# Performance work log

Hardware: AMD Instinct MI355X
Metric: run time of the kernel (lower is better)

## Reference

```python
import jax, jax.numpy as jnp
import numpy as np

D_CH = 2048  # channels
N = 64       # hidden_state
L = 8192     # sequence length
MIN_DELTA, MAX_DELTA = 1e-3, 0.1


def setup_inputs() -> dict:
    key = jax.random.key(0)
    ks = jax.random.split(key, 5)
    X = jax.random.normal(ks[0], (D_CH, L), jnp.float32)
    # kaiming_normal_(nonlinearity='linear'): std = 1/sqrt(fan_in=N)
    A = jax.random.normal(ks[1], (N, N), jnp.float32) * (1.0 / N) ** 0.5
    B = jax.random.normal(ks[2], (N, D_CH), jnp.float32) * (1.0 / N) ** 0.5
    C = jax.random.normal(ks[3], (D_CH, N), jnp.float32)
    Dp = jnp.ones((D_CH,), jnp.float32)
    log_delta = jax.random.uniform(ks[4], (1,), jnp.float32,
                                   float(np.log(MIN_DELTA)), float(np.log(MAX_DELTA)))
    return {"X": X, "A": A, "B": B, "C": C, "Dp": Dp, "log_delta": log_delta}


def reference(X, A, B, C, Dp, log_delta):
    # X: (D, L). Bilinear (Tustin) discretization with dt = exp(log_delta).
    n = A.shape[0]
    delta = jnp.exp(log_delta)[0]
    I = jnp.eye(n, dtype=A.dtype)
    inv = jnp.linalg.inv(I - (delta * 0.5) * A)
    dA = inv @ (I + (delta * 0.5) * A)      # (N, N)
    dB = delta * (inv @ B)                   # (N, D)

    def step(h, x_t):
        # h: (N,), x_t: (D,)
        h = dA @ h + dB @ x_t
        return h, C @ h                      # y_t: (D,)

    h0 = jnp.zeros((n,), X.dtype)
    _, ys = jax.lax.scan(step, h0, X.T)      # ys: (L, D)
    # skip connection y += D * X (per-channel)
    return ys.T + Dp[:, None] * X            # (D, L)
```

## Files before the change

### kernel.cpp

```cpp
#include <hip/hip_runtime.h>
#include <math.h>

#define D_CH 2048
#define LSEQ 8192
#define T1 32
#define NC1 256
#define VSLAB 524288

typedef __attribute__((ext_vector_type(8))) short bf16x8;
typedef __attribute__((ext_vector_type(4))) float f32x4;

__device__ __forceinline__ short f2bf(float x) {
  unsigned u = __float_as_uint(x);
  u += 0x7FFFu + ((u >> 16) & 1);
  return (short)(u >> 16);
}

__device__ __forceinline__ void mmzero(float acc[16]) {
#pragma unroll
  for (int t = 0; t < 16; ++t) acc[t] = 0.f;
}

template <int SZ>
__device__ __forceinline__ void mmld(float acc[16], const float* __restrict__ Z,
                                     int r0, int c0) {
#pragma unroll
  for (int i = 0; i < 4; ++i) {
    float4 z = *(const float4*)&Z[(r0 + i) * SZ + c0];
    acc[i * 4 + 0] = z.x; acc[i * 4 + 1] = z.y;
    acc[i * 4 + 2] = z.z; acc[i * 4 + 3] = z.w;
  }
}

template <int SX, int SY>
__device__ __forceinline__ void mac44(float acc[16], const float* __restrict__ Xb,
                                      const float* __restrict__ Yb, int r0, int c0) {
#pragma unroll 4
  for (int k = 0; k < 64; k += 4) {
    float4 x0 = *(const float4*)&Xb[(r0 + 0) * SX + k];
    float4 x1 = *(const float4*)&Xb[(r0 + 1) * SX + k];
    float4 x2 = *(const float4*)&Xb[(r0 + 2) * SX + k];
    float4 x3 = *(const float4*)&Xb[(r0 + 3) * SX + k];
    float4 y0 = *(const float4*)&Yb[(k + 0) * SY + c0];
    float4 y1 = *(const float4*)&Yb[(k + 1) * SY + c0];
    float4 y2 = *(const float4*)&Yb[(k + 2) * SY + c0];
    float4 y3 = *(const float4*)&Yb[(k + 3) * SY + c0];
#define MROW(i, xi) \
    acc[i * 4 + 0] += xi.x * y0.x + xi.y * y1.x + xi.z * y2.x + xi.w * y3.x; \
    acc[i * 4 + 1] += xi.x * y0.y + xi.y * y1.y + xi.z * y2.y + xi.w * y3.y; \
    acc[i * 4 + 2] += xi.x * y0.z + xi.y * y1.z + xi.z * y2.z + xi.w * y3.z; \
    acc[i * 4 + 3] += xi.x * y0.w + xi.y * y1.w + xi.z * y2.w + xi.w * y3.w;
    MROW(0, x0) MROW(1, x1) MROW(2, x2) MROW(3, x3)
#undef MROW
  }
}

template <int SZ>
__device__ __forceinline__ void mmst(float* Dst, const float acc[16], int r0, int c0) {
#pragma unroll
  for (int i = 0; i < 4; ++i)
    *(float4*)&Dst[(r0 + i) * SZ + c0] =
        make_float4(acc[i * 4 + 0], acc[i * 4 + 1], acc[i * 4 + 2], acc[i * 4 + 3]);
}

__global__ __launch_bounds__(256) void main_kernel(const float* __restrict__ X,
                                                   const float* __restrict__ A,
                                                   const float* __restrict__ B,
                                                   const float* __restrict__ logd,
                                                   float* __restrict__ invdT,
                                                   float* __restrict__ dAg,
                                                   float* __restrict__ V,
                                                   int KS) {
  __shared__ float smem[8704];
  const int tid = threadIdx.x;
  const int lane = tid & 63;
  const int w = tid >> 6;

  if (blockIdx.x == 0) {
    float* bQ = smem;
    float* bP = smem + 4352;
    const int r0 = (tid >> 4) * 4, c0 = (tid & 15) * 4;
    const float delta = expf(logd[0]);
    const float half = 0.5f * delta;
    float accQ[16], accP[16];

    for (int idx = tid; idx < 4096; idx += 256) {
      int i = idx >> 6, j = idx & 63;
      float p = half * A[idx];
      bP[i * 68 + j] = p;
      bQ[i * 68 + j] = p + (i == j ? 1.f : 0.f);
    }
    __syncthreads();
    mmzero(accP); mac44<68, 68>(accP, bP, bP, r0, c0);
    __syncthreads();
    mmst<68>(bP, accP, r0, c0);
    __syncthreads();
#pragma unroll 1
    for (int s = 0; s < 2; ++s) {
      mmld<68>(accQ, bQ, r0, c0);
      mac44<68, 68>(accQ, bP, bQ, r0, c0);
      if (s < 1) { mmzero(accP); mac44<68, 68>(accP, bP, bP, r0, c0); }
      __syncthreads();
      mmst<68>(bQ, accQ, r0, c0);
      if (s < 1) mmst<68>(bP, accP, r0, c0);
      __syncthreads();
    }

    for (int idx = tid; idx < 4096; idx += 256) {
      int n = idx >> 6, m = idx & 63;
      float qv = bQ[n * 68 + m];
      invdT[m * 64 + n] = delta * qv;
      dAg[idx] = 2.f * qv - (n == m ? 1.f : 0.f);
    }
    return;
  }

  const int b = blockIdx.x - 1;
  const int t0 = (b & 255) << 5;
  const int slab = b >> 8;
  const int k0 = slab * KS;
  short* Xs = (short*)smem;
  short* Bs = (short*)smem + 2432;
  const int q = lane >> 4, r = lane & 15;
  const int hi = lane >> 5, tl = lane & 31;
  const int brow = lane >> 3;
  const int bkc = (lane & 7) * 8;
  const int wm = (w & 1) * 16;
  const int wn = (w >> 1) * 32;

  f32x4 acc[2];
#pragma unroll
  for (int j = 0; j < 2; ++j) acc[j] = (f32x4){0.f, 0.f, 0.f, 0.f};

  float xv[8];
  float bv[16];

#define LOADX(KK)                                                              \
  _Pragma("unroll")                                                            \
  for (int j = 0; j < 8; ++j)                                                  \
    xv[j] = X[(size_t)(k0 + (KK) + w * 16 + hi * 8 + j) * LSEQ + t0 + tl];

#define LOADB(KK)                                                              \
  _Pragma("unroll")                                                            \
  for (int pp = 0; pp < 2; ++pp) {                                             \
    int n = pp * 32 + w * 8 + brow;                                            \
    float4 f0 = *(const float4*)&B[(size_t)n * D_CH + k0 + (KK) + bkc];        \
    float4 f1 = *(const float4*)&B[(size_t)n * D_CH + k0 + (KK) + bkc + 4];    \
    bv[pp * 8 + 0] = f0.x; bv[pp * 8 + 1] = f0.y;                              \
    bv[pp * 8 + 2] = f0.z; bv[pp * 8 + 3] = f0.w;                              \
    bv[pp * 8 + 4] = f1.x; bv[pp * 8 + 5] = f1.y;                              \
    bv[pp * 8 + 6] = f1.z; bv[pp * 8 + 7] = f1.w;                              \
  }

  LOADX(0)
  LOADB(0)

  for (int kk = 0; kk < KS; kk += 64) {
    bf16x8 xp;
#pragma unroll
    for (int j = 0; j < 8; ++j) xp[j] = f2bf(xv[j]);
    *(bf16x8*)&Xs[tl * 76 + w * 16 + hi * 8] = xp;
#pragma unroll
    for (int pp = 0; pp < 2; ++pp) {
      bf16x8 bp8;
#pragma unroll
      for (int j = 0; j < 8; ++j) bp8[j] = f2bf(bv[pp * 8 + j]);
      *(bf16x8*)&Bs[(pp * 32 + w * 8 + brow) * 76 + bkc] = bp8;
    }
    __syncthreads();

    if (kk + 64 < KS) {
      LOADX(kk + 64)
      LOADB(kk + 64)
    }

#pragma unroll
    for (int ks = 0; ks < 64; ks += 32) {
      bf16x8 a = *(const bf16x8*)&Xs[(wm + r) * 76 + ks + q * 8];
#pragma unroll
      for (int j = 0; j < 2; ++j) {
        bf16x8 bb = *(const bf16x8*)&Bs[(wn + j * 16 + r) * 76 + ks + q * 8];
        acc[j] = __builtin_amdgcn_mfma_f32_16x16x32_bf16(a, bb, acc[j], 0, 0, 0);
      }
    }
    __syncthreads();
  }
#undef LOADX
#undef LOADB

  float* Vs = V + (size_t)slab * VSLAB;
#pragma unroll
  for (int j = 0; j < 2; ++j)
#pragma unroll
    for (int reg = 0; reg < 4; ++reg)
      Vs[(size_t)(t0 + wm + q * 4 + reg) * 64 + wn + j * 16 + r] = acc[j][reg];
}

__device__ __forceinline__ float matvec_lds(const float* __restrict__ Mrow,
                                            const float* __restrict__ hb, float u) {
  float a0 = u, a1 = 0.f, a2 = 0.f, a3 = 0.f;
#pragma unroll
  for (int jj = 0; jj < 64; jj += 4) {
    float4 m = *(const float4*)&Mrow[jj];
    float4 hv = *(const float4*)&hb[jj];
    a0 += m.x * hv.x;
    a1 += m.y * hv.y;
    a2 += m.z * hv.z;
    a3 += m.w * hv.w;
  }
  return (a0 + a1) + (a2 + a3);
}

__device__ __forceinline__ void stage_mat64(float* Mlds, const float* __restrict__ Mg,
                                            int lane) {
#pragma unroll
  for (int i = 0; i < 16; ++i) {
    int row = i * 4 + (lane >> 4);
    int col = (lane & 15) * 4;
    *(float4*)&Mlds[row * 68 + col] = *(const float4*)&Mg[row * 64 + col];
  }
  __syncthreads();
}

__global__ __launch_bounds__(256) void scan1_kernel(const float* __restrict__ V,
                                                    const float* __restrict__ invdT,
                                                    const float* __restrict__ dA,
                                                    float* __restrict__ U,
                                                    float* __restrict__ S,
                                                    float* __restrict__ dA32g,
                                                    float* __restrict__ dA512g,
                                                    int nslab) {
  __shared__ float smem[13056];
  const int tid = threadIdx.x;
  const int c = blockIdx.x;

  if (c == NC1) {
    float* b0 = smem;
    float* b1 = smem + 4352;
    const int r0 = (tid >> 4) * 4, c0 = (tid & 15) * 4;
    for (int idx = tid; idx < 4096; idx += 256)
      b0[(idx >> 6) * 68 + (idx & 63)] = dA[idx];
    __syncthreads();
    float acc[16];
    float* p = b0; float* q = b1;
    for (int s = 1; s <= 9; ++s) {
      mmzero(acc); mac44<68, 68>(acc, p, p, r0, c0);
      if (s == 5) mmst<64>(dA32g, acc, r0, c0);
      if (s == 9) mmst<64>(dA512g, acc, r0, c0);
      mmst<68>(q, acc, r0, c0);
      __syncthreads();
      float* t = p; p = q; q = t;
    }
    return;
  }

  float* invs = smem;
  float* Vs   = smem + 4096;
  float* Us   = smem + 6144;
  float* hs0  = smem + 8192;
  float* hs1  = smem + 8256;
  float* Md   = smem + 8320;

  for (int idx = tid; idx < 4096; idx += 256) invs[idx] = invdT[idx];
  for (int idx = tid; idx < 4096; idx += 256)
    Md[(idx >> 6) * 68 + (idx & 63)] = dA[idx];
  for (int idx = tid; idx < 2048; idx += 256) {
    float v = 0.f;
    for (int s = 0; s < nslab; ++s) v += V[(size_t)s * VSLAB + (size_t)c * 2048 + idx];
    Vs[idx] = v;
  }
  __syncthreads();

  const int r0 = (tid >> 4) * 2, c0 = (tid & 15) * 4;
  float a0[4] = {0.f, 0.f, 0.f, 0.f}, a1[4] = {0.f, 0.f, 0.f, 0.f};
#pragma unroll 4
  for (int k = 0; k < 64; k += 4) {
    float4 v0 = *(const float4*)&Vs[r0 * 64 + k];
    float4 v1 = *(const float4*)&Vs[(r0 + 1) * 64 + k];
    float4 y0 = *(const float4*)&invs[(k + 0) * 64 + c0];
    float4 y1 = *(const float4*)&invs[(k + 1) * 64 + c0];
    float4 y2 = *(const float4*)&invs[(k + 2) * 64 + c0];
    float4 y3 = *(const float4*)&invs[(k + 3) * 64 + c0];
    a0[0] += v0.x * y0.x + v0.y * y1.x + v0.z * y2.x + v0.w * y3.x;
    a0[1] += v0.x * y0.y + v0.y * y1.y + v0.z * y2.y + v0.w * y3.y;
    a0[2] += v0.x * y0.z + v0.y * y1.z + v0.z * y2.z + v0.w * y3.z;
    a0[3] += v0.x * y0.w + v0.y * y1.w + v0.z * y2.w + v0.w * y3.w;
    a1[0] += v1.x * y0.x + v1.y * y1.x + v1.z * y2.x + v1.w * y3.x;
    a1[1] += v1.x * y0.y + v1.y * y1.y + v1.z * y2.y + v1.w * y3.y;
    a1[2] += v1.x * y0.z + v1.y * y1.z + v1.z * y2.z + v1.w * y3.z;
    a1[3] += v1.x * y0.w + v1.y * y1.w + v1.z * y2.w + v1.w * y3.w;
  }
  *(float4*)&Us[r0 * 64 + c0] = make_float4(a0[0], a0[1], a0[2], a0[3]);
  *(float4*)&Us[(r0 + 1) * 64 + c0] = make_float4(a1[0], a1[1], a1[2], a1[3]);
  *(float4*)&U[(size_t)(c * 32 + r0) * 64 + c0] = make_float4(a0[0], a0[1], a0[2], a0[3]);
  *(float4*)&U[(size_t)(c * 32 + r0 + 1) * 64 + c0] = make_float4(a1[0], a1[1], a1[2], a1[3]);
  __syncthreads();

  if (tid < 64) {
    const float* row = Md + tid * 68;
    float h = 0.f;
    hs0[tid] = 0.f;
    for (int t = 0; t < T1; ++t) {
      float u = Us[t * 64 + tid];
      h = matvec_lds(row, (t & 1) ? hs1 : hs0, u);
      ((t & 1) ? hs0 : hs1)[tid] = h;
    }
    S[c * 64 + tid] = h;
  }
}

__global__ __launch_bounds__(64) void mid1_kernel(const float* __restrict__ S,
                                                  const float* __restrict__ dA32,
                                                  float* __restrict__ S2g) {
  __shared__ float M[64 * 68];
  __shared__ float hs[2][64];
  const int lane = threadIdx.x;
  const int g = blockIdx.x;
  stage_mat64(M, dA32, lane);
  const float* row = M + lane * 68;
  const float* in = S + g * 16 * 64;
  float h = 0.f;
  hs[0][lane] = 0.f;
  for (int t = 0; t < 16; ++t) {
    h = matvec_lds(row, hs[t & 1], in[t * 64 + lane]);
    hs[(t + 1) & 1][lane] = h;
  }
  S2g[g * 64 + lane] = h;
}

__global__ __launch_bounds__(64) void mid2_kernel(const float* __restrict__ S2g,
                                                  const float* __restrict__ dA512,
                                                  float* __restrict__ H2g) {
  __shared__ float M[64 * 68];
  __shared__ float hs[2][64];
  const int lane = threadIdx.x;
  stage_mat64(M, dA512, lane);
  const float* row = M + lane * 68;
  float h = 0.f;
  hs[0][lane] = 0.f;
  for (int t = 0; t < 16; ++t) {
    H2g[t * 64 + lane] = h;
    h = matvec_lds(row, hs[t & 1], S2g[t * 64 + lane]);
    hs[(t + 1) & 1][lane] = h;
  }
}

__global__ __launch_bounds__(64) void mid3_kernel(const float* __restrict__ S,
                                                  const float* __restrict__ dA32,
                                                  const float* __restrict__ H2g,
                                                  float* __restrict__ Hinit) {
  __shared__ float M[64 * 68];
  __shared__ float hs[2][64];
  const int lane = threadIdx.x;
  const int g = blockIdx.x;
  stage_mat64(M, dA32, lane);
  const float* row = M + lane * 68;
  const float* in = S + g * 16 * 64;
  float h = H2g[g * 64 + lane];
  hs[0][lane] = h;
  for (int t = 0; t < 16; ++t) {
    Hinit[(g * 16 + t) * 64 + lane] = h;
    h = matvec_lds(row, hs[t & 1], in[t * 64 + lane]);
    hs[(t + 1) & 1][lane] = h;
  }
}

__global__ __launch_bounds__(64) void scan2_kernel(const float* __restrict__ U,
                                                   const float* __restrict__ dA,
                                                   const float* __restrict__ Hinit,
                                                   float* __restrict__ Ht) {
  __shared__ float M[64 * 68];
  __shared__ float hs[2][64];
  const int tid = threadIdx.x;
  const int c = blockIdx.x;
  stage_mat64(M, dA, tid);
  const float* row = M + tid * 68;
  float h = Hinit[c * 64 + tid];
  hs[0][tid] = h;
  const float* inc = U + (size_t)c * T1 * 64;
  float* outc = Ht + (size_t)c * T1 * 64;
  float up[4];
#pragma unroll
  for (int i = 0; i < 4; ++i) up[i] = inc[i * 64 + tid];

  for (int t = 0; t < T1; ++t) {
    float u = up[t & 3];
    if (t + 4 < T1) up[t & 3] = inc[(t + 4) * 64 + tid];
    h = matvec_lds(row, hs[t & 1], u);
    hs[(t + 1) & 1][tid] = h;
    outc[t * 64 + tid] = h;
  }
}

__global__ __launch_bounds__(256) void out_kernel(const float* __restrict__ X,
                                                  const float* __restrict__ C,
                                                  const float* __restrict__ Dp,
                                                  const float* __restrict__ Ht,
                                                  float* __restrict__ Y) {
  __shared__ short Cs[64 * 76];
  __shared__ short Hs[64 * 76];
  const int tid = threadIdx.x;
  const int lane = tid & 63, w = tid >> 6;
  const int t0 = blockIdx.x * 64;
  const int d0 = blockIdx.y * 64;
  const int q = lane >> 4, r = lane & 15;
  const int brow = lane >> 3, bkc = (lane & 7) * 8;

#pragma unroll
  for (int p = 0; p < 2; ++p) {
    int row = p * 32 + w * 8 + brow;
    float4 c0 = *(const float4*)&C[(size_t)(d0 + row) * 64 + bkc];
    float4 c1 = *(const float4*)&C[(size_t)(d0 + row) * 64 + bkc + 4];
    float4 h0 = *(const float4*)&Ht[(size_t)(t0 + row) * 64 + bkc];
    float4 h1 = *(const float4*)&Ht[(size_t)(t0 + row) * 64 + bkc + 4];
    bf16x8 cv, hv;
    cv[0] = f2bf(c0.x); cv[1] = f2bf(c0.y); cv[2] = f2bf(c0.z); cv[3] = f2bf(c0.w);
    cv[4] = f2bf(c1.x); cv[5] = f2bf(c1.y); cv[6] = f2bf(c1.z); cv[7] = f2bf(c1.w);
    hv[0] = f2bf(h0.x); hv[1] = f2bf(h0.y); hv[2] = f2bf(h0.z); hv[3] = f2bf(h0.w);
    hv[4] = f2bf(h1.x); hv[5] = f2bf(h1.y); hv[6] = f2bf(h1.z); hv[7] = f2bf(h1.w);
    *(bf16x8*)&Cs[row * 76 + bkc] = cv;
    *(bf16x8*)&Hs[row * 76 + bkc] = hv;
  }
  __syncthreads();

  f32x4 acc[4];
#pragma unroll
  for (int j = 0; j < 4; ++j) acc[j] = (f32x4){0.f, 0.f, 0.f, 0.f};
#pragma unroll
  for (int ks = 0; ks < 64; ks += 32) {
    bf16x8 a = *(const bf16x8*)&Cs[(w * 16 + r) * 76 + ks + q * 8];
#pragma unroll
    for (int j = 0; j < 4; ++j) {
      bf16x8 bb = *(const bf16x8*)&Hs[(j * 16 + r) * 76 + ks + q * 8];
      acc[j] = __builtin_amdgcn_mfma_f32_16x16x32_bf16(a, bb, acc[j], 0, 0, 0);
    }
  }

#pragma unroll
  for (int reg = 0; reg < 4; ++reg) {
    int d = d0 + w * 16 + q * 4 + reg;
    float dp = Dp[d];
#pragma unroll
    for (int j = 0; j < 4; ++j) {
      int t = t0 + j * 16 + r;
      size_t off = (size_t)d * LSEQ + t;
      Y[off] = acc[j][reg] + dp * X[off];
    }
  }
}

extern "C" void kernel_launch(void* const* d_in, const int* in_sizes, int n_in,
                              void* d_out, int out_size, void* d_ws, size_t ws_size,
                              hipStream_t stream) {
  const float* X  = (const float*)d_in[0];
  const float* A  = (const float*)d_in[1];
  const float* B  = (const float*)d_in[2];
  const float* Cm = (const float*)d_in[3];
  const float* Dp = (const float*)d_in[4];
  const float* ld = (const float*)d_in[5];
  float* out = (float*)d_out;
  float* ws = (float*)d_ws;

  const size_t need4 =
      (size_t)(16384 + 4 * VSLAB + VSLAB + 16384 + 16384 + 2048) * 4;
  const int nslab = (ws_size >= need4) ? 4 : 2;

  float* invdT = ws;
  float* dA    = ws + 4096;
  float* dA32  = ws + 8192;
  float* dA512 = ws + 12288;
  float* V     = ws + 16384;
  float* U     = V + (size_t)nslab * VSLAB;
  float* S     = U + VSLAB;
  float* Hinit = S + 16384;
  float* S2g   = Hinit + 16384;
  float* H2g   = S2g + 1024;
  float* Ht    = V;

  main_kernel<<<nslab * 256 + 1, 256, 0, stream>>>(X, A, B, ld, invdT, dA, V,
                                                   2048 / nslab);
  scan1_kernel<<<NC1 + 1, 256, 0, stream>>>(V, invdT, dA, U, S, dA32, dA512, nslab);
  mid1_kernel<<<16, 64, 0, stream>>>(S, dA32, S2g);
  mid2_kernel<<<1, 64, 0, stream>>>(S2g, dA512, H2g);
  mid3_kernel<<<16, 64, 0, stream>>>(S, dA32, H2g, Hinit);
  scan2_kernel<<<NC1, 64, 0, stream>>>(U, dA, Hinit, Ht);
  out_kernel<<<dim3(128, 32), 256, 0, stream>>>(X, Cm, Dp, Ht, out);
}
```

Baseline: 240.0 us.

## Restructure projection GEMM: stage 512-wide B chunk in LDS, stream X directly to registers

The X·B projection GEMM now gives each block 64 timesteps instead of 32 and stages a whole 64x512 bf16 slice of B in LDS. The X operand is loaded straight from global memory into MFMA registers with one-step register prefetch, so X no longer goes through LDS. This removes the per-64-k double barriers and the X LDS round trip, and reuses each B slice across more timesteps. The cost is about 65KB of LDS per block, which limits occupancy, and half as many blocks.

Result: no change. 242.6 us (+1.0%).

```diff
diff --git a/kernel.cpp b/kernel.cpp
--- a/kernel.cpp
+++ b/kernel.cpp
@@ -71,12 +71,11 @@
                                                    float* __restrict__ dAg,
                                                    float* __restrict__ V,
                                                    int KS) {
-  __shared__ float smem[8704];
+  __shared__ __align__(16) char smem_raw[66560];
   const int tid = threadIdx.x;
-  const int lane = tid & 63;
-  const int w = tid >> 6;
 
   if (blockIdx.x == 0) {
+    float* smem = (float*)smem_raw;
     float* bQ = smem;
     float* bP = smem + 4352;
     const int r0 = (tid >> 4) * 4, c0 = (tid & 15) * 4;
@@ -115,85 +114,72 @@
     return;
   }
 
+  short* Bs = (short*)smem_raw;
+  const int lane = tid & 63;
+  const int w = tid >> 6;
+  const int q = lane >> 4, r = lane & 15;
   const int b = blockIdx.x - 1;
-  const int t0 = (b & 255) << 5;
-  const int slab = b >> 8;
+  const int t0 = (b & 127) << 6;
+  const int slab = b >> 7;
   const int k0 = slab * KS;
-  short* Xs = (short*)smem;
-  short* Bs = (short*)smem + 2432;
-  const int q = lane >> 4, r = lane & 15;
-  const int hi = lane >> 5, tl = lane & 31;
-  const int brow = lane >> 3;
-  const int bkc = (lane & 7) * 8;
-  const int wm = (w & 1) * 16;
-  const int wn = (w >> 1) * 32;
-
-  f32x4 acc[2];
-#pragma unroll
-  for (int j = 0; j < 2; ++j) acc[j] = (f32x4){0.f, 0.f, 0.f, 0.f};
-
-  float xv[8];
-  float bv[16];
-
-#define LOADX(KK)                                                              \
-  _Pragma("unroll")                                                            \
-  for (int j = 0; j < 8; ++j)                                                  \
-    xv[j] = X[(size_t)(k0 + (KK) + w * 16 + hi * 8 + j) * LSEQ + t0 + tl];
-
-#define LOADB(KK)                                                              \
-  _Pragma("unroll")                                                            \
-  for (int pp = 0; pp < 2; ++pp) {                                             \
-    int n = pp * 32 + w * 8 + brow;                                            \
-    float4 f0 = *(const float4*)&B[(size_t)n * D_CH + k0 + (KK) + bkc];        \
-    float4 f1 = *(const float4*)&B[(size_t)n * D_CH + k0 + (KK) + bkc + 4];    \
-    bv[pp * 8 + 0] = f0.x; bv[pp * 8 + 1] = f0.y;                              \
-    bv[pp * 8 + 2] = f0.z; bv[pp * 8 + 3] = f0.w;                              \
-    bv[pp * 8 + 4] = f1.x; bv[pp * 8 + 5] = f1.y;                              \
-    bv[pp * 8 + 6] = f1.z; bv[pp * 8 + 7] = f1.w;                              \
-  }
-
-  LOADX(0)
-  LOADB(0)
-
-  for (int kk = 0; kk < KS; kk += 64) {
-    bf16x8 xp;
-#pragma unroll
-    for (int j = 0; j < 8; ++j) xp[j] = f2bf(xv[j]);
-    *(bf16x8*)&Xs[tl * 76 + w * 16 + hi * 8] = xp;
-#pragma unroll
-    for (int pp = 0; pp < 2; ++pp) {
-      bf16x8 bp8;
-#pragma unroll
-      for (int j = 0; j < 8; ++j) bp8[j] = f2bf(bv[pp * 8 + j]);
-      *(bf16x8*)&Bs[(pp * 32 + w * 8 + brow) * 76 + bkc] = bp8;
+  const int halves = KS >> 9;
+
+  f32x4 acc[4];
+#pragma unroll
+  for (int j = 0; j < 4; ++j) acc[j] = (f32x4){0.f, 0.f, 0.f, 0.f};
+
+  const int sn = tid >> 2;
+  const int skq = (tid & 3) << 7;
+  const size_t xcol = (size_t)(t0 + w * 16 + r);
+
+  for (int h = 0; h < halves; ++h) {
+    const int kb = k0 + (h << 9);
+
+#pragma unroll 4
+    for (int i = 0; i < 16; ++i) {
+      const float* src = &B[(size_t)sn * D_CH + kb + skq + i * 8];
+      float4 f0 = *(const float4*)src;
+      float4 f1 = *(const float4*)(src + 4);
+      bf16x8 bp;
+      bp[0] = f2bf(f0.x); bp[1] = f2bf(f0.y); bp[2] = f2bf(f0.z); bp[3] = f2bf(f0.w);
+      bp[4] = f2bf(f1.x); bp[5] = f2bf(f1.y); bp[6] = f2bf(f1.z); bp[7] = f2bf(f1.w);
+      *(bf16x8*)&Bs[sn * 520 + skq + i * 8] = bp;
     }
     __syncthreads();
 
-    if (kk + 64 < KS) {
-      LOADX(kk + 64)
-      LOADB(kk + 64)
-    }
-
-#pragma unroll
-    for (int ks = 0; ks < 64; ks += 32) {
-      bf16x8 a = *(const bf16x8*)&Xs[(wm + r) * 76 + ks + q * 8];
-#pragma unroll
-      for (int j = 0; j < 2; ++j) {
-        bf16x8 bb = *(const bf16x8*)&Bs[(wn + j * 16 + r) * 76 + ks + q * 8];
-        acc[j] = __builtin_amdgcn_mfma_f32_16x16x32_bf16(a, bb, acc[j], 0, 0, 0);
+    float xv[8];
+    bf16x8 xa;
+#pragma unroll
+    for (int j = 0; j < 8; ++j)
+      xv[j] = X[(size_t)(kb + q * 8 + j) * LSEQ + xcol];
+#pragma unroll
+    for (int j = 0; j < 8; ++j) xa[j] = f2bf(xv[j]);
+
+    for (int c = 0; c < 16; ++c) {
+      if (c + 1 < 16) {
+#pragma unroll
+        for (int j = 0; j < 8; ++j)
+          xv[j] = X[(size_t)(kb + (c + 1) * 32 + q * 8 + j) * LSEQ + xcol];
       }
-    }
-    __syncthreads();
-  }
-#undef LOADX
-#undef LOADB
+#pragma unroll
+      for (int j = 0; j < 4; ++j) {
+        bf16x8 ba = *(const bf16x8*)&Bs[(j * 16 + r) * 520 + c * 32 + q * 8];
+        acc[j] = __builtin_amdgcn_mfma_f32_16x16x32_bf16(xa, ba, acc[j], 0, 0, 0);
+      }
+      if (c + 1 < 16) {
+#pragma unroll
+        for (int j = 0; j < 8; ++j) xa[j] = f2bf(xv[j]);
+      }
+    }
+    if (h + 1 < halves) __syncthreads();
+  }
 
   float* Vs = V + (size_t)slab * VSLAB;
 #pragma unroll
-  for (int j = 0; j < 2; ++j)
+  for (int j = 0; j < 4; ++j)
 #pragma unroll
     for (int reg = 0; reg < 4; ++reg)
-      Vs[(size_t)(t0 + wm + q * 4 + reg) * 64 + wn + j * 16 + r] = acc[j][reg];
+      Vs[(size_t)(t0 + w * 16 + q * 4 + reg) * 64 + j * 16 + r] = acc[j][reg];
 }
 
 __device__ __forceinline__ float matvec_lds(const float* __restrict__ Mrow,
@@ -477,7 +463,7 @@
   float* H2g   = S2g + 1024;
   float* Ht    = V;
 
-  main_kernel<<<nslab * 256 + 1, 256, 0, stream>>>(X, A, B, ld, invdT, dA, V,
+  main_kernel<<<nslab * 128 + 1, 256, 0, stream>>>(X, A, B, ld, invdT, dA, V,
                                                    2048 / nslab);
   scan1_kernel<<<NC1 + 1, 256, 0, stream>>>(V, invdT, dA, U, S, dA32, dA512, nslab);
   mid1_kernel<<<16, 64, 0, stream>>>(S, dA32, S2g);
```
